# Optimization experiments

Measured on AMD Instinct MI355X. Metric: run time of the kernel, lower is better.

The kernel has to match this reference:

```python
import jax, jax.numpy as jnp
import numpy as np

# Geometry constants fixed by the source's index arithmetic
GRID_P, GRID_Q, NUM_ANCH = 60, 40, 9   # p = (i//9)%60, q = i//(60*9), sr = i%9
N = GRID_P * GRID_Q * NUM_ANCH          # 21600 anchors per image
K = 1000                                # top-K candidates kept before NMS
MAX_BOXES = 18                          # fixed output boxes per image
THRESH = 0.5                            # NMS overlap threshold
BATCH = 64


def setup_inputs() -> dict:
    key = jax.random.key(0)
    k1, k2 = jax.random.split(key)
    x = jax.random.normal(k1, (BATCH, N, 6), dtype=jnp.float32)
    # anchor boxes (x, y, w, h); keep w,h strictly positive and away from 0
    anchor_boxes = jax.random.uniform(k2, (GRID_P, GRID_Q, NUM_ANCH, 4),
                                      dtype=jnp.float32, minval=0.05, maxval=1.0)
    return {"x": x, "anchor_boxes": anchor_boxes}


def _per_sample(ypred, anchors):
    scores, order = jax.lax.top_k(ypred[:, 0], K)          # descending, matches tf.argsort DESC [:1000]
    p = (order // NUM_ANCH) % GRID_P
    q = order // (GRID_P * NUM_ANCH)
    sr = order % NUM_ANCH
    a = anchors[p, q, sr]                                   # [K, 4] (xa, ya, wa, ha)
    regr = ypred[order, 2:6]                                # [K, 4] (dx, dy, dw, dh)
    xc = regr[:, 0] * a[:, 2] + a[:, 0]
    yc = regr[:, 1] * a[:, 3] + a[:, 1]
    w = a[:, 2] * jnp.exp(regr[:, 2])
    h = a[:, 3] * jnp.exp(regr[:, 3])
    cand = jnp.stack([xc, yc, w, h, scores], axis=-1)       # [K, 5] xywh+score

    # xywh -> xyxy for overlap computation (as in non_max_suppression_fast)
    x1 = xc - 0.5 * w; x2 = xc + 0.5 * w
    y1 = yc - 0.5 * h; y2 = yc + 0.5 * h
    area = (x2 - x1) * (y2 - y1)                            # [K]

    # pairwise intersection; overlap[i, j] = inter(i, j) / area(j)  (source divides by
    # the area of the lower-scored candidate, NOT the union -- kept faithfully)
    xx1 = jnp.maximum(x1[:, None], x1[None, :])
    yy1 = jnp.maximum(y1[:, None], y1[None, :])
    xx2 = jnp.minimum(x2[:, None], x2[None, :])
    yy2 = jnp.minimum(y2[:, None], y2[None, :])
    iw = jnp.maximum(0.0, xx2 - xx1)
    ih = jnp.maximum(0.0, yy2 - yy1)
    sup = (iw * ih / area[None, :]) > THRESH                # [K, K] bool

    # greedy NMS over candidates in descending-score order
    jrange = jnp.arange(K)
    def body(i, keep):
        return keep & ~(keep[i] & sup[i] & (jrange > i))
    keep = jax.lax.fori_loop(0, K, body, jnp.ones((K,), dtype=bool))

    # pack first MAX_BOXES kept boxes into fixed-shape output
    ranks = jnp.cumsum(keep) - 1                            # position among kept
    valid = keep & (ranks < MAX_BOXES)
    picked = jnp.zeros((MAX_BOXES, 5), cand.dtype).at[
        jnp.where(valid, ranks, MAX_BOXES)
    ].set(jnp.where(valid[:, None], cand, 0.0), mode='drop')

    # pad with top-scored decoded boxes if fewer than MAX_BOXES survive NMS
    n = jnp.minimum(jnp.sum(keep), MAX_BOXES)
    j = jnp.arange(MAX_BOXES)
    pad = cand[jnp.clip(j - n, 0, K - 1)]
    return jnp.where((j < n)[:, None], picked, pad)         # [MAX_BOXES, 5]


def reference(x, anchor_boxes):
    return jax.vmap(lambda y: _per_sample(y, anchor_boxes))(x)  # [B, 18, 5]
```

## Files before the change

kernel.cpp:

```cpp
#include <hip/hip_runtime.h>

#define GP 60
#define GQ 40
#define NA 9
#define NELEM (GP * GQ * NA)
#define KSEL 1000
#define MAXB 18
#define NT 1024
#define CAP 2048
#define NFULL 21
#define NTAIL (NELEM - NFULL * NT)

typedef unsigned long long ull;

__device__ __forceinline__ unsigned fkey(float f) {
  unsigned u = __float_as_uint(f);
  return (u & 0x80000000u) ? ~u : (u | 0x80000000u);
}

__device__ void select_bucket(const unsigned* hist, unsigned target,
                              volatile unsigned* chunkSuf,
                              unsigned* outB, unsigned* outCnt, unsigned* outAbove) {
  const int tid = threadIdx.x;
  const int w = tid >> 6, l = tid & 63;
  unsigned h1 = hist[w * 128 + 2 * l + 1];
  unsigned s = hist[w * 128 + 2 * l] + h1;
  #pragma unroll
  for (int d = 1; d < 64; d <<= 1) {
    unsigned t = __shfl_down(s, d);
    if (l + d < 64) s += t;
  }
  if (l == 0) chunkSuf[w] = s;
  __syncthreads();
  if (w == 0) {
    unsigned ct = (l < 16) ? chunkSuf[l] : 0u;
    unsigned cs = ct;
    #pragma unroll
    for (int d = 1; d < 16; d <<= 1) {
      unsigned t = __shfl_down(cs, d);
      if (l + d < 16) cs += t;
    }
    if (l < 16) chunkSuf[l] = cs - ct;
  }
  __syncthreads();
  unsigned base = chunkSuf[w];
  unsigned sufE = s + base;
  unsigned sN = __shfl_down(s, 1);
  unsigned sufN = ((l < 63) ? sN : 0u) + base;
  unsigned geOdd = sufN + h1;
  if (sufE >= target && geOdd < target) { *outB = w * 128u + 2u * l;     *outCnt = sufE;  *outAbove = geOdd; }
  if (geOdd >= target && sufN < target) { *outB = w * 128u + 2u * l + 1; *outCnt = geOdd; *outAbove = sufN;  }
  __syncthreads();
}

__global__ __launch_bounds__(NT) void rpn_kernel(
    const float* __restrict__ x, const float* __restrict__ anch,
    float* __restrict__ out) {
  const int b = blockIdx.x;
  const int tid = threadIdx.x;
  const float* xb = x + (size_t)b * NELEM * 6;

  __shared__ unsigned hist[2048];
  __shared__ unsigned chunkSuf[16];
  __shared__ ull selPk[CAP];
  __shared__ float bX1[KSEL], bY1[KSEL], bX2[KSEL], bY2[KSEL], bAr[KSEL];
  __shared__ unsigned sB, sCnt, sAbove;
  __shared__ unsigned baseKey;
  __shared__ unsigned cnt;
  __shared__ int keptRank[MAXB];
  __shared__ int numKept;

  float v[NFULL];
  #pragma unroll
  for (int u = 0; u < NFULL; ++u)
    v[u] = xb[(size_t)(tid + (u << 10)) * 6];
  float vtail = 0.f;
  const bool hastail = tid < NTAIL;
  if (hastail) vtail = xb[(size_t)(tid + NFULL * NT) * 6];

  hist[2 * tid >= 2048 ? 0 : 2 * tid] = 0u;
  hist[2 * tid] = 0u; hist[2 * tid + 1] = 0u;
  __syncthreads();
  #pragma unroll
  for (int u = 0; u < NFULL; ++u)
    atomicAdd(&hist[fkey(v[u]) >> 21], 1u);
  if (hastail) atomicAdd(&hist[fkey(vtail) >> 21], 1u);
  __syncthreads();
  select_bucket(hist, KSEL, chunkSuf, &sB, &sCnt, &sAbove);
  const unsigned b1 = sB, cnt1 = sCnt, above1 = sAbove;

  if (cnt1 <= CAP) {
    if (tid == 0) baseKey = b1 << 21;
  } else {
    hist[2 * tid] = 0u; hist[2 * tid + 1] = 0u;
    __syncthreads();
    #pragma unroll
    for (int u = 0; u < NFULL; ++u) {
      unsigned k = fkey(v[u]);
      if ((k >> 21) == b1) atomicAdd(&hist[(k >> 10) & 0x7FFu], 1u);
    }
    if (hastail) {
      unsigned k = fkey(vtail);
      if ((k >> 21) == b1) atomicAdd(&hist[(k >> 10) & 0x7FFu], 1u);
    }
    __syncthreads();
    select_bucket(hist, KSEL - above1, chunkSuf, &sB, &sCnt, &sAbove);
    if (tid == 0) baseKey = (b1 << 21) | (sB << 10);
  }
  if (tid == 0) cnt = 0u;
  __syncthreads();

  const unsigned TB = baseKey;
  #pragma unroll
  for (int u = 0; u < NFULL; ++u) {
    unsigned k = fkey(v[u]);
    if (k >= TB) {
      unsigned p = atomicAdd(&cnt, 1u);
      unsigned i = (unsigned)(tid + (u << 10));
      if (p < CAP) selPk[p] = ((ull)k << 32) | (unsigned)(~i);
    }
  }
  if (hastail) {
    unsigned k = fkey(vtail);
    if (k >= TB) {
      unsigned p = atomicAdd(&cnt, 1u);
      unsigned i = (unsigned)(tid + NFULL * NT);
      if (p < CAP) selPk[p] = ((ull)k << 32) | (unsigned)(~i);
    }
  }
  __syncthreads();
  const unsigned realCnt = (cnt < CAP) ? cnt : CAP;
  for (unsigned i = realCnt + tid; i < CAP; i += NT) selPk[i] = 0ull;
  __syncthreads();

  for (unsigned k = 2; k <= CAP; k <<= 1) {
    for (unsigned j = k >> 1; j > 0; j >>= 1) {
      unsigned p = (unsigned)tid;
      unsigned vi = ((p & ~(j - 1)) << 1) | (p & (j - 1));
      unsigned li = vi | j;
      ull a = selPk[vi], c = selPk[li];
      bool doswap = ((vi & k) == 0) ? (a < c) : (a > c);
      if (doswap) { selPk[vi] = c; selPk[li] = a; }
      __syncthreads();
    }
  }

  if (tid < KSEL) {
    unsigned idx = ~(unsigned)selPk[tid];
    const float* e = xb + (size_t)idx * 6;
    float r0 = e[2], r1 = e[3], r2 = e[4], r3 = e[5];
    unsigned pp = (idx / 9u) % 60u;
    unsigned qq = idx / 540u;
    unsigned sr = idx % 9u;
    const float* ap = anch + (((pp * 40u + qq) * 9u + sr) * 4u);
    float ax = ap[0], ay = ap[1], aw = ap[2], ah = ap[3];
    float xc = r0 * aw + ax;
    float yc = r1 * ah + ay;
    float w = aw * expf(r2);
    float h = ah * expf(r3);
    float x1 = xc - 0.5f * w, x2 = xc + 0.5f * w;
    float y1 = yc - 0.5f * h, y2 = yc + 0.5f * h;
    bX1[tid] = x1; bY1[tid] = y1; bX2[tid] = x2; bY2[tid] = y2;
    bAr[tid] = (x2 - x1) * (y2 - y1);
  }
  __syncthreads();

  if (tid < 64) {
    const int lane = tid;
    int nk = 0;
    float kx1 = 0.f, ky1 = 0.f, kx2 = 0.f, ky2 = 0.f;
    int krank = -1;
    for (int base = 0; base < KSEL && nk < MAXB; base += 64) {
      int c = base + lane;
      bool alive = (c < KSEL);
      int cc = alive ? c : 0;
      float x1 = bX1[cc], y1 = bY1[cc], x2 = bX2[cc], y2 = bY2[cc], ar = bAr[cc];
      for (int i = 0; i < nk; ++i) {
        float px1 = __shfl(kx1, i), py1 = __shfl(ky1, i);
        float px2 = __shfl(kx2, i), py2 = __shfl(ky2, i);
        float iw = fmaxf(fminf(x2, px2) - fmaxf(x1, px1), 0.f);
        float ih = fmaxf(fminf(y2, py2) - fmaxf(y1, py1), 0.f);
        if (iw * ih / ar > 0.5f) alive = false;
      }
      unsigned long long m = __ballot(alive);
      while (m) {
        int i = __builtin_ctzll(m);
        float px1 = __shfl(x1, i), py1 = __shfl(y1, i);
        float px2 = __shfl(x2, i), py2 = __shfl(y2, i);
        if (lane == nk) { kx1 = px1; ky1 = py1; kx2 = px2; ky2 = py2; krank = base + i; }
        ++nk;
        if (nk >= MAXB) break;
        if (alive && lane != i) {
          float iw = fmaxf(fminf(x2, px2) - fmaxf(x1, px1), 0.f);
          float ih = fmaxf(fminf(y2, py2) - fmaxf(y1, py1), 0.f);
          if (iw * ih / ar > 0.5f) alive = false;
        }
        if (lane == i) alive = false;
        m = __ballot(alive);
      }
    }
    if (lane == 0) numKept = nk;
    if (lane < nk) keptRank[lane] = krank;
  }
  __syncthreads();

  const int n = numKept;
  if (tid < MAXB) {
    int j = tid;
    int r = (j < n) ? keptRank[j] : (j - n);
    unsigned idx = ~(unsigned)selPk[r];
    const float* e = xb + (size_t)idx * 6;
    float sc = e[0];
    float r0 = e[2], r1 = e[3], r2 = e[4], r3 = e[5];
    unsigned pp = (idx / 9u) % 60u;
    unsigned qq = idx / 540u;
    unsigned sr = idx % 9u;
    const float* ap = anch + (((pp * 40u + qq) * 9u + sr) * 4u);
    float ax = ap[0], ay = ap[1], aw = ap[2], ah = ap[3];
    float xc = r0 * aw + ax;
    float yc = r1 * ah + ay;
    float w = aw * expf(r2);
    float h = ah * expf(r3);
    float* o = out + b * (MAXB * 5) + j * 5;
    o[0] = xc; o[1] = yc; o[2] = w; o[3] = h; o[4] = sc;
  }
}

extern "C" void kernel_launch(void* const* d_in, const int* in_sizes, int n_in,
                              void* d_out, int out_size, void* d_ws, size_t ws_size,
                              hipStream_t stream) {
  const float* x = (const float*)d_in[0];
  const float* anch = (const float*)d_in[1];
  float* out = (float*)d_out;
  const int B = in_sizes[0] / (NELEM * 6);
  rpn_kernel<<<dim3(B), dim3(NT), 0, stream>>>(x, anch, out);
}
```

Baseline: 66.87 us.

## Vectorize score loads via float4 and move small bitonic stages into wavefront shuffles

Scores are now read by streaming the per-image buffer as coalesced float4 loads and picking the score lane from each vector, replacing strided scalar loads kept in registers. The input is re-read for each histogram or select pass rather than cached in registers. The bitonic sort also does every stage with stride below 128 in registers using shuffles within a 64-lane wavefront. Only the larger strides go through shared memory, which removes most of the per-step __syncthreads barriers. The cost is more global traffic, since the whole row is read including unused columns, plus extra modulo arithmetic per element.

```diff
diff --git a/kernel.cpp b/kernel.cpp
--- a/kernel.cpp
+++ b/kernel.cpp
@@ -1,15 +1,13 @@
 #include <hip/hip_runtime.h>
 
-#define GP 60
-#define GQ 40
-#define NA 9
-#define NELEM (GP * GQ * NA)
+#define NELEM 21600
 #define KSEL 1000
 #define MAXB 18
 #define NT 1024
 #define CAP 2048
-#define NFULL 21
-#define NTAIL (NELEM - NFULL * NT)
+#define NQ (NELEM * 6 / 4)
+#define NQF (NQ / NT)
+#define NQT (NQ - NQF * NT)
 
 typedef unsigned long long ull;
 
@@ -59,6 +57,7 @@
   const int b = blockIdx.x;
   const int tid = threadIdx.x;
   const float* xb = x + (size_t)b * NELEM * 6;
+  const float4* xq = (const float4*)xb;
 
   __shared__ unsigned hist[2048];
   __shared__ unsigned chunkSuf[16];
@@ -70,62 +69,84 @@
   __shared__ int keptRank[MAXB];
   __shared__ int numKept;
 
-  float v[NFULL];
-  #pragma unroll
-  for (int u = 0; u < NFULL; ++u)
-    v[u] = xb[(size_t)(tid + (u << 10)) * 6];
-  float vtail = 0.f;
-  const bool hastail = tid < NTAIL;
-  if (hastail) vtail = xb[(size_t)(tid + NFULL * NT) * 6];
-
-  hist[2 * tid >= 2048 ? 0 : 2 * tid] = 0u;
   hist[2 * tid] = 0u; hist[2 * tid + 1] = 0u;
   __syncthreads();
-  #pragma unroll
-  for (int u = 0; u < NFULL; ++u)
-    atomicAdd(&hist[fkey(v[u]) >> 21], 1u);
-  if (hastail) atomicAdd(&hist[fkey(vtail) >> 21], 1u);
+
+  #pragma unroll 4
+  for (int k = 0; k < NQF; ++k) {
+    int g = tid + (k << 10);
+    float4 v = xq[g];
+    int r = g % 3;
+    if (r == 0)      atomicAdd(&hist[fkey(v.x) >> 21], 1u);
+    else if (r == 1) atomicAdd(&hist[fkey(v.z) >> 21], 1u);
+  }
+  if (tid < NQT) {
+    int g = tid + (NQF << 10);
+    float4 v = xq[g];
+    int r = g % 3;
+    if (r == 0)      atomicAdd(&hist[fkey(v.x) >> 21], 1u);
+    else if (r == 1) atomicAdd(&hist[fkey(v.z) >> 21], 1u);
+  }
   __syncthreads();
   select_bucket(hist, KSEL, chunkSuf, &sB, &sCnt, &sAbove);
   const unsigned b1 = sB, cnt1 = sCnt, above1 = sAbove;
 
   if (cnt1 <= CAP) {
-    if (tid == 0) baseKey = b1 << 21;
+    if (tid == 0) { baseKey = b1 << 21; cnt = 0u; }
   } else {
     hist[2 * tid] = 0u; hist[2 * tid + 1] = 0u;
     __syncthreads();
-    #pragma unroll
-    for (int u = 0; u < NFULL; ++u) {
-      unsigned k = fkey(v[u]);
-      if ((k >> 21) == b1) atomicAdd(&hist[(k >> 10) & 0x7FFu], 1u);
-    }
-    if (hastail) {
-      unsigned k = fkey(vtail);
-      if ((k >> 21) == b1) atomicAdd(&hist[(k >> 10) & 0x7FFu], 1u);
+    #pragma unroll 4
+    for (int k = 0; k < NQF; ++k) {
+      int g = tid + (k << 10);
+      float4 v = xq[g];
+      int r = g % 3;
+      if (r != 2) {
+        unsigned kk = fkey(r == 0 ? v.x : v.z);
+        if ((kk >> 21) == b1) atomicAdd(&hist[(kk >> 10) & 0x7FFu], 1u);
+      }
+    }
+    if (tid < NQT) {
+      int g = tid + (NQF << 10);
+      float4 v = xq[g];
+      int r = g % 3;
+      if (r != 2) {
+        unsigned kk = fkey(r == 0 ? v.x : v.z);
+        if ((kk >> 21) == b1) atomicAdd(&hist[(kk >> 10) & 0x7FFu], 1u);
+      }
     }
     __syncthreads();
     select_bucket(hist, KSEL - above1, chunkSuf, &sB, &sCnt, &sAbove);
-    if (tid == 0) baseKey = (b1 << 21) | (sB << 10);
-  }
-  if (tid == 0) cnt = 0u;
+    if (tid == 0) { baseKey = (b1 << 21) | (sB << 10); cnt = 0u; }
+  }
   __syncthreads();
 
   const unsigned TB = baseKey;
-  #pragma unroll
-  for (int u = 0; u < NFULL; ++u) {
-    unsigned k = fkey(v[u]);
-    if (k >= TB) {
-      unsigned p = atomicAdd(&cnt, 1u);
-      unsigned i = (unsigned)(tid + (u << 10));
-      if (p < CAP) selPk[p] = ((ull)k << 32) | (unsigned)(~i);
-    }
-  }
-  if (hastail) {
-    unsigned k = fkey(vtail);
-    if (k >= TB) {
-      unsigned p = atomicAdd(&cnt, 1u);
-      unsigned i = (unsigned)(tid + NFULL * NT);
-      if (p < CAP) selPk[p] = ((ull)k << 32) | (unsigned)(~i);
+  #pragma unroll 4
+  for (int k = 0; k < NQF; ++k) {
+    int g = tid + (k << 10);
+    float4 v = xq[g];
+    int r = g % 3;
+    if (r != 2) {
+      unsigned kk = fkey(r == 0 ? v.x : v.z);
+      if (kk >= TB) {
+        unsigned p = atomicAdd(&cnt, 1u);
+        unsigned idx = 2u * (unsigned)(g / 3) + (r == 1 ? 1u : 0u);
+        if (p < CAP) selPk[p] = ((ull)kk << 32) | (unsigned)(~idx);
+      }
+    }
+  }
+  if (tid < NQT) {
+    int g = tid + (NQF << 10);
+    float4 v = xq[g];
+    int r = g % 3;
+    if (r != 2) {
+      unsigned kk = fkey(r == 0 ? v.x : v.z);
+      if (kk >= TB) {
+        unsigned p = atomicAdd(&cnt, 1u);
+        unsigned idx = 2u * (unsigned)(g / 3) + (r == 1 ? 1u : 0u);
+        if (p < CAP) selPk[p] = ((ull)kk << 32) | (unsigned)(~idx);
+      }
     }
   }
   __syncthreads();
@@ -133,14 +154,52 @@
   for (unsigned i = realCnt + tid; i < CAP; i += NT) selPk[i] = 0ull;
   __syncthreads();
 
-  for (unsigned k = 2; k <= CAP; k <<= 1) {
-    for (unsigned j = k >> 1; j > 0; j >>= 1) {
-      unsigned p = (unsigned)tid;
-      unsigned vi = ((p & ~(j - 1)) << 1) | (p & (j - 1));
-      unsigned li = vi | j;
-      ull a = selPk[vi], c = selPk[li];
-      bool doswap = ((vi & k) == 0) ? (a < c) : (a > c);
-      if (doswap) { selPk[vi] = c; selPk[li] = a; }
+  {
+    const int w = tid >> 6, L = tid & 63;
+    const int ea = (w << 7) | (L << 1);
+    ull a = selPk[ea], bb = selPk[ea + 1];
+    #pragma unroll
+    for (unsigned k = 2; k <= 128; k <<= 1) {
+      #pragma unroll
+      for (unsigned j = k >> 1; j >= 2; j >>= 1) {
+        bool up = ((ea & k) == 0);
+        bool lower = ((ea & j) == 0);
+        bool takeMax = (up == lower);
+        ull oa = __shfl_xor(a, (int)(j >> 1));
+        ull ob = __shfl_xor(bb, (int)(j >> 1));
+        a  = takeMax ? (a  > oa ? a  : oa) : (a  < oa ? a  : oa);
+        bb = takeMax ? (bb > ob ? bb : ob) : (bb < ob ? bb : ob);
+      }
+      bool up = ((ea & k) == 0);
+      ull mx = a > bb ? a : bb, mn = a > bb ? bb : a;
+      a = up ? mx : mn; bb = up ? mn : mx;
+    }
+    selPk[ea] = a; selPk[ea + 1] = bb;
+    __syncthreads();
+    for (unsigned k = 256; k <= 2048; k <<= 1) {
+      for (unsigned j = k >> 1; j >= 128; j >>= 1) {
+        unsigned p = (unsigned)tid;
+        unsigned vi = ((p & ~(j - 1)) << 1) | (p & (j - 1));
+        unsigned li = vi | j;
+        ull av = selPk[vi], cv = selPk[li];
+        bool doswap = ((vi & k) == 0) ? (av < cv) : (av > cv);
+        if (doswap) { selPk[vi] = cv; selPk[li] = av; }
+        __syncthreads();
+      }
+      a = selPk[ea]; bb = selPk[ea + 1];
+      bool up = (((unsigned)(w << 7) & k) == 0);
+      #pragma unroll
+      for (unsigned j = 64; j >= 2; j >>= 1) {
+        bool lower = ((ea & j) == 0);
+        bool takeMax = (up == lower);
+        ull oa = __shfl_xor(a, (int)(j >> 1));
+        ull ob = __shfl_xor(bb, (int)(j >> 1));
+        a  = takeMax ? (a  > oa ? a  : oa) : (a  < oa ? a  : oa);
+        bb = takeMax ? (bb > ob ? bb : ob) : (bb < ob ? bb : ob);
+      }
+      ull mx = a > bb ? a : bb, mn = a > bb ? bb : a;
+      a = up ? mx : mn; bb = up ? mn : mx;
+      selPk[ea] = a; selPk[ea + 1] = bb;
       __syncthreads();
     }
   }
```

Result: slower. 80.68 us (+20.7%).

## Sort bitonic stages within wavefronts via shuffles and overlap histogram init

Applied to the files above, without the earlier changes.

Replaces the shared-memory bitonic sort's small-stride stages with register-resident compare-exchanges using wave-level xor shuffles, with each thread holding two elements. This cuts most of the block-wide barriers and LDS round trips, since only strides of 128 and above still go through shared memory. It also moves histogram zeroing ahead of the score loads, and pins the loaded values in registers with an empty asm so they are not rematerialized. Smaller changes load the regression deltas as float2, recover the score from the packed sort key instead of re-reading global memory, and add a launch-bounds occupancy hint.

```diff
diff --git a/kernel.cpp b/kernel.cpp
--- a/kernel.cpp
+++ b/kernel.cpp
@@ -1,9 +1,6 @@
 #include <hip/hip_runtime.h>
 
-#define GP 60
-#define GQ 40
-#define NA 9
-#define NELEM (GP * GQ * NA)
+#define NELEM 21600
 #define KSEL 1000
 #define MAXB 18
 #define NT 1024
@@ -16,6 +13,10 @@
 __device__ __forceinline__ unsigned fkey(float f) {
   unsigned u = __float_as_uint(f);
   return (u & 0x80000000u) ? ~u : (u | 0x80000000u);
+}
+__device__ __forceinline__ float unfkey(unsigned k) {
+  unsigned u = (k & 0x80000000u) ? (k ^ 0x80000000u) : ~k;
+  return __uint_as_float(u);
 }
 
 __device__ void select_bucket(const unsigned* hist, unsigned target,
@@ -53,7 +54,7 @@
   __syncthreads();
 }
 
-__global__ __launch_bounds__(NT) void rpn_kernel(
+__global__ __launch_bounds__(NT, 4) void rpn_kernel(
     const float* __restrict__ x, const float* __restrict__ anch,
     float* __restrict__ out) {
   const int b = blockIdx.x;
@@ -70,50 +71,55 @@
   __shared__ int keptRank[MAXB];
   __shared__ int numKept;
 
-  float v[NFULL];
+  hist[2 * tid] = 0u; hist[2 * tid + 1] = 0u;
+
+  float sv[NFULL];
   #pragma unroll
   for (int u = 0; u < NFULL; ++u)
-    v[u] = xb[(size_t)(tid + (u << 10)) * 6];
-  float vtail = 0.f;
+    sv[u] = xb[(size_t)(tid + (u << 10)) * 6];
+  float stail = 0.f;
   const bool hastail = tid < NTAIL;
-  if (hastail) vtail = xb[(size_t)(tid + NFULL * NT) * 6];
-
-  hist[2 * tid >= 2048 ? 0 : 2 * tid] = 0u;
-  hist[2 * tid] = 0u; hist[2 * tid + 1] = 0u;
-  __syncthreads();
+  if (hastail) stail = xb[(size_t)(tid + NFULL * NT) * 6];
+  asm volatile("" :
+      "+v"(sv[0]), "+v"(sv[1]), "+v"(sv[2]), "+v"(sv[3]), "+v"(sv[4]),
+      "+v"(sv[5]), "+v"(sv[6]), "+v"(sv[7]), "+v"(sv[8]), "+v"(sv[9]),
+      "+v"(sv[10]), "+v"(sv[11]), "+v"(sv[12]), "+v"(sv[13]), "+v"(sv[14]),
+      "+v"(sv[15]), "+v"(sv[16]), "+v"(sv[17]), "+v"(sv[18]), "+v"(sv[19]),
+      "+v"(sv[20]), "+v"(stail));
+  __syncthreads();
+
   #pragma unroll
   for (int u = 0; u < NFULL; ++u)
-    atomicAdd(&hist[fkey(v[u]) >> 21], 1u);
-  if (hastail) atomicAdd(&hist[fkey(vtail) >> 21], 1u);
+    atomicAdd(&hist[fkey(sv[u]) >> 21], 1u);
+  if (hastail) atomicAdd(&hist[fkey(stail) >> 21], 1u);
   __syncthreads();
   select_bucket(hist, KSEL, chunkSuf, &sB, &sCnt, &sAbove);
   const unsigned b1 = sB, cnt1 = sCnt, above1 = sAbove;
 
   if (cnt1 <= CAP) {
-    if (tid == 0) baseKey = b1 << 21;
+    if (tid == 0) { baseKey = b1 << 21; cnt = 0u; }
   } else {
     hist[2 * tid] = 0u; hist[2 * tid + 1] = 0u;
     __syncthreads();
     #pragma unroll
     for (int u = 0; u < NFULL; ++u) {
-      unsigned k = fkey(v[u]);
+      unsigned k = fkey(sv[u]);
       if ((k >> 21) == b1) atomicAdd(&hist[(k >> 10) & 0x7FFu], 1u);
     }
     if (hastail) {
-      unsigned k = fkey(vtail);
+      unsigned k = fkey(stail);
       if ((k >> 21) == b1) atomicAdd(&hist[(k >> 10) & 0x7FFu], 1u);
     }
     __syncthreads();
     select_bucket(hist, KSEL - above1, chunkSuf, &sB, &sCnt, &sAbove);
-    if (tid == 0) baseKey = (b1 << 21) | (sB << 10);
-  }
-  if (tid == 0) cnt = 0u;
+    if (tid == 0) { baseKey = (b1 << 21) | (sB << 10); cnt = 0u; }
+  }
   __syncthreads();
 
   const unsigned TB = baseKey;
   #pragma unroll
   for (int u = 0; u < NFULL; ++u) {
-    unsigned k = fkey(v[u]);
+    unsigned k = fkey(sv[u]);
     if (k >= TB) {
       unsigned p = atomicAdd(&cnt, 1u);
       unsigned i = (unsigned)(tid + (u << 10));
@@ -121,7 +127,7 @@
     }
   }
   if (hastail) {
-    unsigned k = fkey(vtail);
+    unsigned k = fkey(stail);
     if (k >= TB) {
       unsigned p = atomicAdd(&cnt, 1u);
       unsigned i = (unsigned)(tid + NFULL * NT);
@@ -133,31 +139,69 @@
   for (unsigned i = realCnt + tid; i < CAP; i += NT) selPk[i] = 0ull;
   __syncthreads();
 
-  for (unsigned k = 2; k <= CAP; k <<= 1) {
-    for (unsigned j = k >> 1; j > 0; j >>= 1) {
-      unsigned p = (unsigned)tid;
-      unsigned vi = ((p & ~(j - 1)) << 1) | (p & (j - 1));
-      unsigned li = vi | j;
-      ull a = selPk[vi], c = selPk[li];
-      bool doswap = ((vi & k) == 0) ? (a < c) : (a > c);
-      if (doswap) { selPk[vi] = c; selPk[li] = a; }
+  {
+    const int w = tid >> 6, L = tid & 63;
+    const int ea = (w << 7) | (L << 1);
+    ull a = selPk[ea], bb = selPk[ea + 1];
+    #pragma unroll
+    for (unsigned k = 2; k <= 128; k <<= 1) {
+      #pragma unroll
+      for (unsigned j = k >> 1; j >= 2; j >>= 1) {
+        bool up = ((ea & k) == 0);
+        bool lower = ((ea & j) == 0);
+        bool takeMax = (up == lower);
+        ull oa = __shfl_xor(a, (int)(j >> 1));
+        ull ob = __shfl_xor(bb, (int)(j >> 1));
+        a  = takeMax ? (a  > oa ? a  : oa) : (a  < oa ? a  : oa);
+        bb = takeMax ? (bb > ob ? bb : ob) : (bb < ob ? bb : ob);
+      }
+      bool up = ((ea & k) == 0);
+      ull mx = a > bb ? a : bb, mn = a > bb ? bb : a;
+      a = up ? mx : mn; bb = up ? mn : mx;
+    }
+    selPk[ea] = a; selPk[ea + 1] = bb;
+    __syncthreads();
+    for (unsigned k = 256; k <= 2048; k <<= 1) {
+      for (unsigned j = k >> 1; j >= 128; j >>= 1) {
+        unsigned p = (unsigned)tid;
+        unsigned vi = ((p & ~(j - 1)) << 1) | (p & (j - 1));
+        unsigned li = vi | j;
+        ull av = selPk[vi], cv = selPk[li];
+        bool doswap = ((vi & k) == 0) ? (av < cv) : (av > cv);
+        if (doswap) { selPk[vi] = cv; selPk[li] = av; }
+        __syncthreads();
+      }
+      a = selPk[ea]; bb = selPk[ea + 1];
+      bool up = (((unsigned)(w << 7) & k) == 0);
+      #pragma unroll
+      for (unsigned j = 64; j >= 2; j >>= 1) {
+        bool lower = ((ea & j) == 0);
+        bool takeMax = (up == lower);
+        ull oa = __shfl_xor(a, (int)(j >> 1));
+        ull ob = __shfl_xor(bb, (int)(j >> 1));
+        a  = takeMax ? (a  > oa ? a  : oa) : (a  < oa ? a  : oa);
+        bb = takeMax ? (bb > ob ? bb : ob) : (bb < ob ? bb : ob);
+      }
+      ull mx = a > bb ? a : bb, mn = a > bb ? bb : a;
+      a = up ? mx : mn; bb = up ? mn : mx;
+      selPk[ea] = a; selPk[ea + 1] = bb;
       __syncthreads();
     }
   }
 
   if (tid < KSEL) {
     unsigned idx = ~(unsigned)selPk[tid];
-    const float* e = xb + (size_t)idx * 6;
-    float r0 = e[2], r1 = e[3], r2 = e[4], r3 = e[5];
+    const float2* e2 = (const float2*)(xb + (size_t)idx * 6 + 2);
+    float2 ra = e2[0], rb = e2[1];
     unsigned pp = (idx / 9u) % 60u;
     unsigned qq = idx / 540u;
     unsigned sr = idx % 9u;
     const float* ap = anch + (((pp * 40u + qq) * 9u + sr) * 4u);
     float ax = ap[0], ay = ap[1], aw = ap[2], ah = ap[3];
-    float xc = r0 * aw + ax;
-    float yc = r1 * ah + ay;
-    float w = aw * expf(r2);
-    float h = ah * expf(r3);
+    float xc = ra.x * aw + ax;
+    float yc = ra.y * ah + ay;
+    float w = aw * expf(rb.x);
+    float h = ah * expf(rb.y);
     float x1 = xc - 0.5f * w, x2 = xc + 0.5f * w;
     float y1 = yc - 0.5f * h, y2 = yc + 0.5f * h;
     bX1[tid] = x1; bY1[tid] = y1; bX2[tid] = x2; bY2[tid] = y2;
@@ -208,19 +252,20 @@
   if (tid < MAXB) {
     int j = tid;
     int r = (j < n) ? keptRank[j] : (j - n);
-    unsigned idx = ~(unsigned)selPk[r];
-    const float* e = xb + (size_t)idx * 6;
-    float sc = e[0];
-    float r0 = e[2], r1 = e[3], r2 = e[4], r3 = e[5];
+    ull pk = selPk[r];
+    unsigned idx = ~(unsigned)pk;
+    float sc = unfkey((unsigned)(pk >> 32));
+    const float2* e2 = (const float2*)(xb + (size_t)idx * 6 + 2);
+    float2 ra = e2[0], rb = e2[1];
     unsigned pp = (idx / 9u) % 60u;
     unsigned qq = idx / 540u;
     unsigned sr = idx % 9u;
     const float* ap = anch + (((pp * 40u + qq) * 9u + sr) * 4u);
     float ax = ap[0], ay = ap[1], aw = ap[2], ah = ap[3];
-    float xc = r0 * aw + ax;
-    float yc = r1 * ah + ay;
-    float w = aw * expf(r2);
-    float h = ah * expf(r3);
+    float xc = ra.x * aw + ax;
+    float yc = ra.y * ah + ay;
+    float w = aw * expf(rb.x);
+    float h = ah * expf(rb.y);
     float* o = out + b * (MAXB * 5) + j * 5;
     o[0] = xc; o[1] = yc; o[2] = w; o[3] = h; o[4] = sc;
   }
```

Result: faster. 63.94 us (-4.4%).
